# Kernel tuning notes

Measured on AMD Instinct MI355X. Metric: run time of the kernel, lower is better.

## Reference

```python
import jax, jax.numpy as jnp
import numpy as np

N = 50000   # nodes
E = 800000  # edges per timestep
T = 2
IN_C = 128
HID = 128


def gcn_conv(x, src, dst, W, b):
    """PyG GCNConv: add self-loops, symmetric normalization, linear, scatter-add, bias."""
    n = x.shape[0]
    loop = jnp.arange(n, dtype=src.dtype)
    s = jnp.concatenate([src, loop])  # [E+N]
    d = jnp.concatenate([dst, loop])
    h = x @ W                          # [N, H]
    deg = jax.ops.segment_sum(jnp.ones_like(d, dtype=x.dtype), d, num_segments=n)
    dinv = jnp.where(deg > 0, jax.lax.rsqrt(deg), 0.0)
    norm = dinv[s] * dinv[d]           # [E+N]
    msg = h[s] * norm[:, None]         # gather + scale
    out = jax.ops.segment_sum(msg, d, num_segments=n)  # scatter-add
    return out + b


def setup_inputs() -> dict:
    key = jax.random.key(0)
    ks = jax.random.split(key, 6)
    x_seq = jax.random.normal(ks[0], (T, N, IN_C), dtype=jnp.float32)
    edge_indices = jax.random.randint(ks[1], (T, 2, E), 0, N, dtype=jnp.int64)
    W1 = jax.random.normal(ks[2], (IN_C, HID), dtype=jnp.float32) * (1.0 / np.sqrt(IN_C))
    b1 = jnp.zeros((HID,), dtype=jnp.float32)
    W2 = jax.random.normal(ks[3], (HID, HID), dtype=jnp.float32) * (1.0 / np.sqrt(HID))
    b2 = jnp.zeros((HID,), dtype=jnp.float32)
    Wc = jax.random.normal(ks[4], (HID, 1), dtype=jnp.float32) * (1.0 / np.sqrt(HID))
    bc = jnp.zeros((1,), dtype=jnp.float32)
    return {"x_seq": x_seq, "edge_indices": edge_indices, "W1": W1, "b1": b1,
            "W2": W2, "b2": b2, "Wc": Wc, "bc": bc}


def reference(x_seq, edge_indices, W1, b1, W2, b2, Wc, bc):
    outputs = []
    for t in range(T):  # small fixed timestep loop, as in original
        x_t = x_seq[t]
        src = edge_indices[t, 0]
        dst = edge_indices[t, 1]
        h = jax.nn.relu(gcn_conv(x_t, src, dst, W1, b1))
        # dropout is inference-identity (eval mode)
        h = gcn_conv(h, src, dst, W2, b2)
        outputs.append(h)
    final = outputs[-1]
    importance_out = (final @ Wc + bc).squeeze(-1)  # [N]
    return (importance_out, *outputs)
```

## Files before the change

kernel.cpp:

```cpp
#include <hip/hip_runtime.h>
#include <hip/hip_bf16.h>

typedef unsigned int u32;
typedef unsigned short u16;
typedef unsigned long long u64;
typedef __bf16 bf16x8 __attribute__((ext_vector_type(8)));
typedef short short8 __attribute__((ext_vector_type(8)));
typedef float floatx4 __attribute__((ext_vector_type(4)));

__device__ inline float b2f(u16 b) { return __uint_as_float((u32)b << 16); }
__device__ inline float lo2f(u32 p) { return __uint_as_float(p << 16); }
__device__ inline float hi2f(u32 p) { return __uint_as_float(p & 0xffff0000u); }
__device__ inline u16 f2bs(float f) {
    __hip_bfloat16 h = __float2bfloat16(f);
    return *reinterpret_cast<u16*>(&h);
}
__device__ inline float ldext(const void* p, int fl, int i) {
    return fl ? ((const float*)p)[i] : b2f(((const u16*)p)[i]);
}

__global__ __launch_bounds__(64) void detect_kernel(const int* __restrict__ eb,
                                                    const u32* __restrict__ xw,
                                                    int* __restrict__ flags,
                                                    int S, int n) {
    __shared__ int sh[64 * 3];
    int lane = threadIdx.x & 63;
    int zc = 0, explo = 0;
#pragma unroll
    for (int r = 0; r < 4; ++r) {
        int i = 64 * r + lane;
        zc += (eb[2 * i + 1] == 0) ? 1 : 0;
        u32 w = xw[i];
        int e = (int)((w >> 7) & 0xFF);
        explo += (e >= 96 && e <= 140) ? 1 : 0;
    }
    sh[lane] = zc;
    sh[64 + lane] = explo;
    __syncthreads();
    int fl = 0;
    {
        int z = 0;
        for (int j = 0; j < 64; ++j) z += sh[j];
        fl = (z > 200) ? 1 : 0;
    }
    int vc = 0;
#pragma unroll
    for (int r = 0; r < 4; ++r) {
        int li = S / 2 + 64 * r + lane;
        int v = fl ? eb[2 * li] : eb[li];
        vc += ((unsigned)v < (unsigned)n) ? 1 : 0;
    }
    sh[128 + lane] = vc;
    __syncthreads();
    if (lane == 0) {
        int vtot = 0, etot = 0;
        for (int j = 0; j < 64; ++j) vtot += sh[128 + j];
        for (int j = 0; j < 64; ++j) etot += sh[64 + j];
        flags[0] = fl;
        flags[1] = (etot >= 192) ? 0 : 1;
        flags[2] = (vtot >= 240) ? (S / 4) : (S / 8);
    }
}

__device__ inline int load_edge(const int* eb, int fl, int idx) {
    return eb[fl ? (idx << 1) : idx];
}

#define PCHUNK 4096
__global__ __launch_bounds__(256) void part_kernel(const int* __restrict__ eb,
                                                   const int* __restrict__ flags,
                                                   int* __restrict__ bkcnt,
                                                   u64* __restrict__ pairs,
                                                   int n, int shift, int capP) {
    __shared__ int cnt[512];
    __shared__ int gbase[512];
    const int E = flags[2];
    const int fl = flags[0];
    const int nbuk = (2 * n + (1 << shift) - 1) >> shift;
    const int tid = threadIdx.x;
    for (int i = tid; i < nbuk; i += 256) cnt[i] = 0;
    __syncthreads();
    const int e0 = blockIdx.x * PCHUNK;
    u32 sv[16]; int gv[16], rk[16];
#pragma unroll
    for (int j = 0; j < 16; ++j) {
        int e = e0 + j * 256 + tid;
        u32 gs = 0; int g = -1;
        if (e < 2 * E) {
            int t = (e >= E) ? 1 : 0;
            int le = e - t * E;
            gs = (u32)(t * n) + (u32)load_edge(eb, fl, t * 2 * E + le);
            unsigned du = (unsigned)load_edge(eb, fl, t * 2 * E + E + le);
            if (du < (unsigned)n) g = t * n + (int)du;
        }
        sv[j] = gs;
        gv[j] = g;
        rk[j] = (g >= 0) ? atomicAdd(&cnt[g >> shift], 1) : 0;
    }
    __syncthreads();
    for (int b = tid; b < nbuk; b += 256) {
        int c = cnt[b];
        gbase[b] = c ? atomicAdd(&bkcnt[b], c) : 0;
    }
    __syncthreads();
#pragma unroll
    for (int j = 0; j < 16; ++j) {
        if (gv[j] >= 0) {
            int b = gv[j] >> shift;
            int idx = gbase[b] + rk[j];
            if (idx < capP)
                pairs[(size_t)b * capP + idx] =
                    ((u64)(u32)gv[j] << 32) | sv[j];
        }
    }
}

__global__ __launch_bounds__(256) void scat_kernel(const u64* __restrict__ pairs,
                                                   const int* __restrict__ bkcnt,
                                                   int* __restrict__ deg,
                                                   int* __restrict__ off,
                                                   float* __restrict__ dinv,
                                                   int* __restrict__ ssrc,
                                                   int n2, int shift, int capP) {
    __shared__ int hist[1024];
    __shared__ int lscan[256];
    const int b = blockIdx.x;
    const int d0 = b << shift;
    if (d0 >= n2) return;
    int nn = (1 << shift);
    if (d0 + nn > n2) nn = n2 - d0;
    const int tid = threadIdx.x;
    for (int j = tid; j < nn; j += 256) hist[j] = 0;
    __syncthreads();
    int cnt = bkcnt[b];
    if (cnt > capP) cnt = capP;
    const int gb = b * capP;
    const u64* pb = pairs + (size_t)gb;
    for (int i = tid; i < cnt; i += 256) {
        unsigned dl = (unsigned)(int)(pb[i] >> 32) - (unsigned)d0;
        if (dl < (unsigned)nn) atomicAdd(&hist[dl], 1);
    }
    __syncthreads();
    int base4 = tid * 4;
    int s0 = 0, s1 = 0, s2 = 0, s3 = 0;
    if (base4 < nn) {
        s0 = hist[base4];
        s1 = (base4 + 1 < nn) ? hist[base4 + 1] : 0;
        s2 = (base4 + 2 < nn) ? hist[base4 + 2] : 0;
        s3 = (base4 + 3 < nn) ? hist[base4 + 3] : 0;
    }
    int tsum = s0 + s1 + s2 + s3;
    lscan[tid] = tsum;
    __syncthreads();
    int val = tsum;
    for (int o = 1; o < 256; o <<= 1) {
        int add = (tid >= o) ? lscan[tid - o] : 0;
        __syncthreads();
        val += add;
        lscan[tid] = val;
        __syncthreads();
    }
    int texcl = val - tsum;
    if (base4 < nn) {
        int g = d0 + base4;
        int o0 = gb + texcl;
        deg[g] = s0; off[g] = o0; dinv[g] = rsqrtf((float)(s0 + 1));
        hist[base4] = o0;
        if (base4 + 1 < nn) {
            int o1 = o0 + s0;
            deg[g + 1] = s1; off[g + 1] = o1; dinv[g + 1] = rsqrtf((float)(s1 + 1));
            hist[base4 + 1] = o1;
        }
        if (base4 + 2 < nn) {
            int o2 = o0 + s0 + s1;
            deg[g + 2] = s2; off[g + 2] = o2; dinv[g + 2] = rsqrtf((float)(s2 + 1));
            hist[base4 + 2] = o2;
        }
        if (base4 + 3 < nn) {
            int o3 = o0 + s0 + s1 + s2;
            deg[g + 3] = s3; off[g + 3] = o3; dinv[g + 3] = rsqrtf((float)(s3 + 1));
            hist[base4 + 3] = o3;
        }
    }
    __syncthreads();
    const int limit = gb + cnt;
    for (int i = tid; i < cnt; i += 256) {
        u64 p = pb[i];
        unsigned dl = (unsigned)(int)(p >> 32) - (unsigned)d0;
        if (dl < (unsigned)nn) {
            int pos = atomicAdd(&hist[dl], 1);
            if (pos < limit) ssrc[pos] = (int)(u32)p;
        }
    }
}

__global__ __launch_bounds__(256) void prep_w(const void* __restrict__ W1,
                                              const void* __restrict__ W2,
                                              const int* __restrict__ flags,
                                              u16* __restrict__ W1t,
                                              u16* __restrict__ W2t) {
    int tid = blockIdx.x * 256 + threadIdx.x;
    if (tid < 2 * 128 * 128) {
        int which = tid >> 14;
        int r = tid & 16383;
        const void* W = which ? W2 : W1;
        u16* Wt = which ? W2t : W1t;
        int c = r >> 7, k = r & 127;
        Wt[c * 128 + k] = f2bs(ldext(W, flags[1], k * 128 + c));
    }
}

__global__ __launch_bounds__(256) void gemm_mfma(const void* __restrict__ Xv,
                                                 int x_ext,
                                                 const u16* __restrict__ Wt,
                                                 const int* __restrict__ flags,
                                                 const float* __restrict__ dinv,
                                                 u16* __restrict__ hs, int n) {
    __shared__ u16 Ws[128 * 136];
    {
        u32* wsu = (u32*)Ws;
        const u32* wtu = (const u32*)Wt;
        for (int i = threadIdx.x; i < 128 * 64; i += 256) {
            int c = i >> 6, kk = i & 63;
            wsu[c * 68 + kk] = wtu[i];
        }
    }
    __syncthreads();

    const int wave = threadIdx.x >> 6;
    const int lane = threadIdx.x & 63;
    const int m = lane & 15;
    const int quad = lane >> 4;
    const int node0 = blockIdx.x * 64 + wave * 16;
    if (node0 >= n) return;

    const int xf32 = x_ext ? flags[1] : 0;
    int va = node0 + m;
    if (va > n - 1) va = n - 1;

    floatx4 acc[8];
#pragma unroll
    for (int t = 0; t < 8; ++t) acc[t] = (floatx4){0.f, 0.f, 0.f, 0.f};

#pragma unroll
    for (int ks = 0; ks < 4; ++ks) {
        bf16x8 a;
        if (xf32) {
            const float* Xf = (const float*)Xv + (size_t)va * 128 + ks * 32 + quad * 8;
            float4 x0 = *(const float4*)Xf;
            float4 x1 = *(const float4*)(Xf + 4);
            short8 as;
            as[0] = (short)f2bs(x0.x); as[1] = (short)f2bs(x0.y);
            as[2] = (short)f2bs(x0.z); as[3] = (short)f2bs(x0.w);
            as[4] = (short)f2bs(x1.x); as[5] = (short)f2bs(x1.y);
            as[6] = (short)f2bs(x1.z); as[7] = (short)f2bs(x1.w);
            a = __builtin_bit_cast(bf16x8, as);
        } else {
            const u16* Xb = (const u16*)Xv + (size_t)va * 128 + ks * 32 + quad * 8;
            a = *(const bf16x8*)Xb;
        }
#pragma unroll
        for (int t = 0; t < 8; ++t) {
            const bf16x8 b = *(const bf16x8*)(Ws + (16 * t + m) * 136 + ks * 32 + quad * 8);
            acc[t] = __builtin_amdgcn_mfma_f32_16x16x32_bf16(a, b, acc[t], 0, 0, 0);
        }
    }

#pragma unroll
    for (int r = 0; r < 4; ++r) {
        int v = node0 + quad * 4 + r;
        if (v < n) {
            float dv = dinv[v];
#pragma unroll
            for (int t = 0; t < 8; ++t)
                hs[(size_t)v * 128 + 16 * t + m] = f2bs(acc[t][r] * dv);
        }
    }
}

__global__ __launch_bounds__(256) void gather_kernel(const u16* __restrict__ hs,
                                                     const int* __restrict__ off,
                                                     const int* __restrict__ deg,
                                                     const int* __restrict__ ssrc,
                                                     const float* __restrict__ dinv,
                                                     const void* __restrict__ bias,
                                                     const int* __restrict__ flags,
                                                     float* __restrict__ outf,
                                                     u16* __restrict__ outb,
                                                     const void* __restrict__ Wc,
                                                     const void* __restrict__ bc,
                                                     float* __restrict__ imp,
                                                     int n2, int half, int relu) {
    int w = (blockIdx.x * 256 + threadIdx.x) >> 6;
    int lane = threadIdx.x & 63;
    if (w >= n2) return;

    const u32* hsu = (const u32*)hs;
    u32 p = hsu[(size_t)w * 64 + lane];
    float ax = lo2f(p), ay = hi2f(p);
    int i = __builtin_amdgcn_readfirstlane(off[w]);
    int end = i + __builtin_amdgcn_readfirstlane(deg[w]);
    unsigned nm1 = (unsigned)(n2 - 1);

    float bx = 0.f, by = 0.f, cx = 0.f, cy = 0.f, dx = 0.f, dy = 0.f;
    for (; i + 8 <= end; i += 8) {
        unsigned s0 = (unsigned)ssrc[i];     if (s0 > nm1) s0 = 0;
        unsigned s1 = (unsigned)ssrc[i + 1]; if (s1 > nm1) s1 = 0;
        unsigned s2 = (unsigned)ssrc[i + 2]; if (s2 > nm1) s2 = 0;
        unsigned s3 = (unsigned)ssrc[i + 3]; if (s3 > nm1) s3 = 0;
        unsigned s4 = (unsigned)ssrc[i + 4]; if (s4 > nm1) s4 = 0;
        unsigned s5 = (unsigned)ssrc[i + 5]; if (s5 > nm1) s5 = 0;
        unsigned s6 = (unsigned)ssrc[i + 6]; if (s6 > nm1) s6 = 0;
        unsigned s7 = (unsigned)ssrc[i + 7]; if (s7 > nm1) s7 = 0;
        u32 v0 = hsu[(size_t)s0 * 64 + lane];
        u32 v1 = hsu[(size_t)s1 * 64 + lane];
        u32 v2 = hsu[(size_t)s2 * 64 + lane];
        u32 v3 = hsu[(size_t)s3 * 64 + lane];
        u32 v4 = hsu[(size_t)s4 * 64 + lane];
        u32 v5 = hsu[(size_t)s5 * 64 + lane];
        u32 v6 = hsu[(size_t)s6 * 64 + lane];
        u32 v7 = hsu[(size_t)s7 * 64 + lane];
        ax += lo2f(v0); ay += hi2f(v0);
        bx += lo2f(v1); by += hi2f(v1);
        cx += lo2f(v2); cy += hi2f(v2);
        dx += lo2f(v3); dy += hi2f(v3);
        ax += lo2f(v4); ay += hi2f(v4);
        bx += lo2f(v5); by += hi2f(v5);
        cx += lo2f(v6); cy += hi2f(v6);
        dx += lo2f(v7); dy += hi2f(v7);
    }
    for (; i + 4 <= end; i += 4) {
        unsigned s0 = (unsigned)ssrc[i];     if (s0 > nm1) s0 = 0;
        unsigned s1 = (unsigned)ssrc[i + 1]; if (s1 > nm1) s1 = 0;
        unsigned s2 = (unsigned)ssrc[i + 2]; if (s2 > nm1) s2 = 0;
        unsigned s3 = (unsigned)ssrc[i + 3]; if (s3 > nm1) s3 = 0;
        u32 v0 = hsu[(size_t)s0 * 64 + lane];
        u32 v1 = hsu[(size_t)s1 * 64 + lane];
        u32 v2 = hsu[(size_t)s2 * 64 + lane];
        u32 v3 = hsu[(size_t)s3 * 64 + lane];
        ax += lo2f(v0); ay += hi2f(v0);
        bx += lo2f(v1); by += hi2f(v1);
        cx += lo2f(v2); cy += hi2f(v2);
        dx += lo2f(v3); dy += hi2f(v3);
    }
    for (; i < end; ++i) {
        unsigned s = (unsigned)ssrc[i];
        if (s > nm1) s = 0;
        u32 v = hsu[(size_t)s * 64 + lane];
        ax += lo2f(v);
        ay += hi2f(v);
    }
    ax += bx + cx + dx;
    ay += by + cy + dy;

    int ffl = flags[1];
    float dv = dinv[w];
    float o0 = dv * ax + ldext(bias, ffl, 2 * lane);
    float o1 = dv * ay + ldext(bias, ffl, 2 * lane + 1);
    if (relu) {
        o0 = fmaxf(o0, 0.f);
        o1 = fmaxf(o1, 0.f);
    }
    if (outf) ((float2*)outf)[(size_t)w * 64 + lane] = make_float2(o0, o1);
    else ((u32*)outb)[(size_t)w * 64 + lane] = (u32)f2bs(o0) | ((u32)f2bs(o1) << 16);

    if (imp && w >= half) {
        float cb = o0 * ldext(Wc, ffl, 2 * lane) + o1 * ldext(Wc, ffl, 2 * lane + 1);
        cb += __shfl_xor(cb, 32);
        cb += __shfl_xor(cb, 16);
        cb += __shfl_xor(cb, 8);
        cb += __shfl_xor(cb, 4);
        cb += __shfl_xor(cb, 2);
        cb += __shfl_xor(cb, 1);
        if (lane == 0) imp[w - half] = cb + ldext(bc, ffl, 0);
    }
}

extern "C" void kernel_launch(void* const* d_in, const int* in_sizes, int n_in,
                              void* d_out, int out_size, void* d_ws, size_t ws_size,
                              hipStream_t stream) {
    const int T = 2, C = 128;
    const int N = in_sizes[0] / (T * C);
    const int S = in_sizes[1];
    const int Emax = S / 4;
    const int N2 = 2 * N;
    (void)Emax;

    const void* x_seq = d_in[0];
    const int* edges = (const int*)d_in[1];
    const void* W1 = d_in[2];
    const void* b1 = d_in[3];
    const void* W2 = d_in[4];
    const void* b2 = d_in[5];
    const void* Wc = d_in[6];
    const void* bc = d_in[7];

    float* out = (float*)d_out;
    float* R = out + N;

    char* p = (char*)d_ws;
    auto alloc = [&](size_t bytes) {
        char* r = p;
        p += (bytes + 255) & ~(size_t)255;
        return r;
    };
    int* flags = (int*)alloc(256);
    int* deg = (int*)alloc((size_t)N2 * 4);
    int* off = (int*)alloc((size_t)N2 * 4);
    float* dinv = (float*)alloc((size_t)N2 * 4);
    int* bkcnt = (int*)alloc(512 * 4);

    int shift = 8;
    while ((((N2 + (1 << shift) - 1) >> shift) > 512) && shift < 10) ++shift;
    const int NBUK = (N2 + (1 << shift) - 1) >> shift;
    const size_t aliasBytes = (size_t)2 * N2 * C * 2;
    const int capP = (int)(aliasBytes / (8 * (size_t)NBUK));

    int* ssrc = (int*)alloc((size_t)NBUK * capP * 4);
    u16* W1t = (u16*)alloc(128 * 128 * 2);
    u16* W2t = (u16*)alloc(128 * 128 * 2);
    u16* hsb = (u16*)alloc((size_t)N2 * C * 2);
    u16* hmb = (u16*)alloc((size_t)N2 * C * 2);
    u64* pairs = (u64*)hsb;

    const int gP = (2 * Emax + PCHUNK - 1) / PCHUNK;
    const int gN2 = (N2 + 3) / 4;
    const int gG2 = (N2 + 63) / 64;
    const int gW = (2 * 128 * 128 + 255) / 256;

    detect_kernel<<<1, 64, 0, stream>>>(edges, (const u32*)x_seq, flags, S, N);
    prep_w<<<gW, 256, 0, stream>>>(W1, W2, flags, W1t, W2t);

    hipMemsetAsync(bkcnt, 0, 512 * 4, stream);
    part_kernel<<<gP, 256, 0, stream>>>(edges, flags, bkcnt, pairs, N, shift, capP);
    scat_kernel<<<NBUK, 256, 0, stream>>>(pairs, bkcnt, deg, off, dinv,
                                          ssrc, N2, shift, capP);

    gemm_mfma<<<gG2, 256, 0, stream>>>(x_seq, 1, W1t, flags, dinv, hsb, N2);
    gather_kernel<<<gN2, 256, 0, stream>>>(hsb, off, deg, ssrc, dinv, b1, flags,
                                           (float*)nullptr, hmb,
                                           nullptr, nullptr, (float*)nullptr,
                                           N2, N, 1);

    gemm_mfma<<<gG2, 256, 0, stream>>>(hmb, 0, W2t, flags, dinv, hsb, N2);
    gather_kernel<<<gN2, 256, 0, stream>>>(hsb, off, deg, ssrc, dinv, b2, flags,
                                           R, (u16*)nullptr,
                                           Wc, bc, out,
                                           N2, N, 0);
}
```

Before: 293.2 us.

## Replace CSR adjacency with fixed 32-slot padded ELL plus overflow list

Neighbor lists become a fixed 32-slot-per-node ELL layout padded with a sentinel that maps to an all-zero row, with a separate overflow array for nodes of higher degree. The gather then loads all 32 indices at once with vector loads and issues 32 unconditional row loads, with no offset lookup or loop tail. Weight preparation moves into extra blocks of the partition kernel, and bucket-counter zeroing moves into the detect kernel, which removes a launch and a memset. The cost is wasted gathers on padded slots, since average degree is about 16, plus the extra work of writing sentinels.

```diff
diff --git a/kernel.cpp b/kernel.cpp
--- a/kernel.cpp
+++ b/kernel.cpp
@@ -8,6 +8,8 @@
 typedef short short8 __attribute__((ext_vector_type(8)));
 typedef float floatx4 __attribute__((ext_vector_type(4)));
 
+#define SENT 0x7FFFFFFF
+
 __device__ inline float b2f(u16 b) { return __uint_as_float((u32)b << 16); }
 __device__ inline float lo2f(u32 p) { return __uint_as_float(p << 16); }
 __device__ inline float hi2f(u32 p) { return __uint_as_float(p & 0xffff0000u); }
@@ -22,9 +24,13 @@
 __global__ __launch_bounds__(64) void detect_kernel(const int* __restrict__ eb,
                                                     const u32* __restrict__ xw,
                                                     int* __restrict__ flags,
+                                                    int* __restrict__ bkcnt,
+                                                    int* __restrict__ ovfcur,
                                                     int S, int n) {
     __shared__ int sh[64 * 3];
     int lane = threadIdx.x & 63;
+    for (int j = lane; j < 512; j += 64) bkcnt[j] = 0;
+    if (lane == 0) *ovfcur = 0;
     int zc = 0, explo = 0;
 #pragma unroll
     for (int r = 0; r < 4; ++r) {
@@ -71,9 +77,26 @@
                                                    const int* __restrict__ flags,
                                                    int* __restrict__ bkcnt,
                                                    u64* __restrict__ pairs,
-                                                   int n, int shift, int capP) {
+                                                   int n, int shift, int capP,
+                                                   int gP,
+                                                   const void* __restrict__ W1,
+                                                   const void* __restrict__ W2,
+                                                   u16* __restrict__ W1t,
+                                                   u16* __restrict__ W2t) {
     __shared__ int cnt[512];
     __shared__ int gbase[512];
+    if ((int)blockIdx.x >= gP) {
+        int tid = (blockIdx.x - gP) * 256 + threadIdx.x;
+        if (tid < 2 * 128 * 128) {
+            int which = tid >> 14;
+            int r = tid & 16383;
+            const void* W = which ? W2 : W1;
+            u16* Wt = which ? W2t : W1t;
+            int c = r >> 7, k = r & 127;
+            Wt[c * 128 + k] = f2bs(ldext(W, flags[1], k * 128 + c));
+        }
+        return;
+    }
     const int E = flags[2];
     const int fl = flags[0];
     const int nbuk = (2 * n + (1 << shift) - 1) >> shift;
@@ -118,95 +141,51 @@
 __global__ __launch_bounds__(256) void scat_kernel(const u64* __restrict__ pairs,
                                                    const int* __restrict__ bkcnt,
                                                    int* __restrict__ deg,
-                                                   int* __restrict__ off,
                                                    float* __restrict__ dinv,
                                                    int* __restrict__ ssrc,
+                                                   int* __restrict__ ovf,
+                                                   int* __restrict__ ovfoff,
+                                                   int* __restrict__ ovfcur,
                                                    int n2, int shift, int capP) {
     __shared__ int hist[1024];
-    __shared__ int lscan[256];
+    __shared__ int cur[1024];
     const int b = blockIdx.x;
     const int d0 = b << shift;
     if (d0 >= n2) return;
     int nn = (1 << shift);
     if (d0 + nn > n2) nn = n2 - d0;
     const int tid = threadIdx.x;
-    for (int j = tid; j < nn; j += 256) hist[j] = 0;
+    for (int j = tid; j < nn; j += 256) { hist[j] = 0; cur[j] = 0; }
     __syncthreads();
     int cnt = bkcnt[b];
     if (cnt > capP) cnt = capP;
-    const int gb = b * capP;
-    const u64* pb = pairs + (size_t)gb;
+    const u64* pb = pairs + (size_t)b * capP;
     for (int i = tid; i < cnt; i += 256) {
         unsigned dl = (unsigned)(int)(pb[i] >> 32) - (unsigned)d0;
         if (dl < (unsigned)nn) atomicAdd(&hist[dl], 1);
     }
     __syncthreads();
-    int base4 = tid * 4;
-    int s0 = 0, s1 = 0, s2 = 0, s3 = 0;
-    if (base4 < nn) {
-        s0 = hist[base4];
-        s1 = (base4 + 1 < nn) ? hist[base4 + 1] : 0;
-        s2 = (base4 + 2 < nn) ? hist[base4 + 2] : 0;
-        s3 = (base4 + 3 < nn) ? hist[base4 + 3] : 0;
-    }
-    int tsum = s0 + s1 + s2 + s3;
-    lscan[tid] = tsum;
-    __syncthreads();
-    int val = tsum;
-    for (int o = 1; o < 256; o <<= 1) {
-        int add = (tid >= o) ? lscan[tid - o] : 0;
-        __syncthreads();
-        val += add;
-        lscan[tid] = val;
-        __syncthreads();
-    }
-    int texcl = val - tsum;
-    if (base4 < nn) {
-        int g = d0 + base4;
-        int o0 = gb + texcl;
-        deg[g] = s0; off[g] = o0; dinv[g] = rsqrtf((float)(s0 + 1));
-        hist[base4] = o0;
-        if (base4 + 1 < nn) {
-            int o1 = o0 + s0;
-            deg[g + 1] = s1; off[g + 1] = o1; dinv[g + 1] = rsqrtf((float)(s1 + 1));
-            hist[base4 + 1] = o1;
-        }
-        if (base4 + 2 < nn) {
-            int o2 = o0 + s0 + s1;
-            deg[g + 2] = s2; off[g + 2] = o2; dinv[g + 2] = rsqrtf((float)(s2 + 1));
-            hist[base4 + 2] = o2;
-        }
-        if (base4 + 3 < nn) {
-            int o3 = o0 + s0 + s1 + s2;
-            deg[g + 3] = s3; off[g + 3] = o3; dinv[g + 3] = rsqrtf((float)(s3 + 1));
-            hist[base4 + 3] = o3;
-        }
-    }
-    __syncthreads();
-    const int limit = gb + cnt;
+    for (int j = tid; j < nn; j += 256) {
+        int d = hist[j];
+        int g = d0 + j;
+        deg[g] = d;
+        dinv[g] = rsqrtf((float)(d + 1));
+        if (d > 32) ovfoff[g] = atomicAdd(ovfcur, d - 32);
+    }
+    for (int idx = tid; idx < nn * 32; idx += 256) {
+        int node = idx >> 5, slot = idx & 31;
+        if (slot >= hist[node]) ssrc[(size_t)(d0 + node) * 32 + slot] = SENT;
+    }
+    __syncthreads();
     for (int i = tid; i < cnt; i += 256) {
         u64 p = pb[i];
         unsigned dl = (unsigned)(int)(p >> 32) - (unsigned)d0;
         if (dl < (unsigned)nn) {
-            int pos = atomicAdd(&hist[dl], 1);
-            if (pos < limit) ssrc[pos] = (int)(u32)p;
-        }
-    }
-}
-
-__global__ __launch_bounds__(256) void prep_w(const void* __restrict__ W1,
-                                              const void* __restrict__ W2,
-                                              const int* __restrict__ flags,
-                                              u16* __restrict__ W1t,
-                                              u16* __restrict__ W2t) {
-    int tid = blockIdx.x * 256 + threadIdx.x;
-    if (tid < 2 * 128 * 128) {
-        int which = tid >> 14;
-        int r = tid & 16383;
-        const void* W = which ? W2 : W1;
-        u16* Wt = which ? W2t : W1t;
-        int c = r >> 7, k = r & 127;
-        Wt[c * 128 + k] = f2bs(ldext(W, flags[1], k * 128 + c));
+            int g = d0 + (int)dl;
+            int slot = atomicAdd(&cur[dl], 1);
+            if (slot < 32) ssrc[(size_t)g * 32 + slot] = (int)(u32)p;
+            else ovf[ovfoff[g] + slot - 32] = (int)(u32)p;
+        }
     }
 }
 
@@ -216,6 +195,8 @@
                                                  const int* __restrict__ flags,
                                                  const float* __restrict__ dinv,
                                                  u16* __restrict__ hs, int n) {
+    if (blockIdx.x == 0 && threadIdx.x < 64)
+        ((u32*)hs)[(size_t)n * 64 + threadIdx.x] = 0;
     __shared__ u16 Ws[128 * 136];
     {
         u32* wsu = (u32*)Ws;
@@ -279,9 +260,10 @@
 }
 
 __global__ __launch_bounds__(256) void gather_kernel(const u16* __restrict__ hs,
-                                                     const int* __restrict__ off,
                                                      const int* __restrict__ deg,
                                                      const int* __restrict__ ssrc,
+                                                     const int* __restrict__ ovf,
+                                                     const int* __restrict__ ovfoff,
                                                      const float* __restrict__ dinv,
                                                      const void* __restrict__ bias,
                                                      const int* __restrict__ flags,
@@ -291,70 +273,92 @@
                                                      const void* __restrict__ bc,
                                                      float* __restrict__ imp,
                                                      int n2, int half, int relu) {
-    int w = (blockIdx.x * 256 + threadIdx.x) >> 6;
-    int lane = threadIdx.x & 63;
+    const int lane = threadIdx.x & 63;
+    int w = __builtin_amdgcn_readfirstlane((blockIdx.x * 256 + threadIdx.x) >> 6);
     if (w >= n2) return;
 
     const u32* hsu = (const u32*)hs;
-    u32 p = hsu[(size_t)w * 64 + lane];
-    float ax = lo2f(p), ay = hi2f(p);
-    int i = __builtin_amdgcn_readfirstlane(off[w]);
-    int end = i + __builtin_amdgcn_readfirstlane(deg[w]);
-    unsigned nm1 = (unsigned)(n2 - 1);
-
+    const unsigned nm1 = (unsigned)(n2 - 1);
+    const unsigned zrow = (unsigned)n2;
+
+    const int dg = __builtin_amdgcn_readfirstlane(deg[w]);
+    const int* sp = ssrc + (size_t)w * 32;
+
+    int4 q0 = *(const int4*)(sp);
+    int4 q1 = *(const int4*)(sp + 4);
+    int4 q2 = *(const int4*)(sp + 8);
+    int4 q3 = *(const int4*)(sp + 12);
+    int4 q4 = *(const int4*)(sp + 16);
+    int4 q5 = *(const int4*)(sp + 20);
+    int4 q6 = *(const int4*)(sp + 24);
+    int4 q7 = *(const int4*)(sp + 28);
+    u32 pself = hsu[(size_t)w * 64 + lane];
+
+#define CLAMP(x) ((unsigned)(x) > nm1 ? zrow : (unsigned)(x))
+    unsigned s00 = CLAMP(q0.x), s01 = CLAMP(q0.y), s02 = CLAMP(q0.z), s03 = CLAMP(q0.w);
+    unsigned s04 = CLAMP(q1.x), s05 = CLAMP(q1.y), s06 = CLAMP(q1.z), s07 = CLAMP(q1.w);
+    unsigned s08 = CLAMP(q2.x), s09 = CLAMP(q2.y), s10 = CLAMP(q2.z), s11 = CLAMP(q2.w);
+    unsigned s12 = CLAMP(q3.x), s13 = CLAMP(q3.y), s14 = CLAMP(q3.z), s15 = CLAMP(q3.w);
+    unsigned s16 = CLAMP(q4.x), s17 = CLAMP(q4.y), s18 = CLAMP(q4.z), s19 = CLAMP(q4.w);
+    unsigned s20 = CLAMP(q5.x), s21 = CLAMP(q5.y), s22 = CLAMP(q5.z), s23 = CLAMP(q5.w);
+    unsigned s24 = CLAMP(q6.x), s25 = CLAMP(q6.y), s26 = CLAMP(q6.z), s27 = CLAMP(q6.w);
+    unsigned s28 = CLAMP(q7.x), s29 = CLAMP(q7.y), s30 = CLAMP(q7.z), s31 = CLAMP(q7.w);
+#undef CLAMP
+
+    float ax = lo2f(pself), ay = hi2f(pself);
     float bx = 0.f, by = 0.f, cx = 0.f, cy = 0.f, dx = 0.f, dy = 0.f;
-    for (; i + 8 <= end; i += 8) {
-        unsigned s0 = (unsigned)ssrc[i];     if (s0 > nm1) s0 = 0;
-        unsigned s1 = (unsigned)ssrc[i + 1]; if (s1 > nm1) s1 = 0;
-        unsigned s2 = (unsigned)ssrc[i + 2]; if (s2 > nm1) s2 = 0;
-        unsigned s3 = (unsigned)ssrc[i + 3]; if (s3 > nm1) s3 = 0;
-        unsigned s4 = (unsigned)ssrc[i + 4]; if (s4 > nm1) s4 = 0;
-        unsigned s5 = (unsigned)ssrc[i + 5]; if (s5 > nm1) s5 = 0;
-        unsigned s6 = (unsigned)ssrc[i + 6]; if (s6 > nm1) s6 = 0;
-        unsigned s7 = (unsigned)ssrc[i + 7]; if (s7 > nm1) s7 = 0;
-        u32 v0 = hsu[(size_t)s0 * 64 + lane];
-        u32 v1 = hsu[(size_t)s1 * 64 + lane];
-        u32 v2 = hsu[(size_t)s2 * 64 + lane];
-        u32 v3 = hsu[(size_t)s3 * 64 + lane];
-        u32 v4 = hsu[(size_t)s4 * 64 + lane];
-        u32 v5 = hsu[(size_t)s5 * 64 + lane];
-        u32 v6 = hsu[(size_t)s6 * 64 + lane];
-        u32 v7 = hsu[(size_t)s7 * 64 + lane];
-        ax += lo2f(v0); ay += hi2f(v0);
-        bx += lo2f(v1); by += hi2f(v1);
-        cx += lo2f(v2); cy += hi2f(v2);
-        dx += lo2f(v3); dy += hi2f(v3);
-        ax += lo2f(v4); ay += hi2f(v4);
-        bx += lo2f(v5); by += hi2f(v5);
-        cx += lo2f(v6); cy += hi2f(v6);
-        dx += lo2f(v7); dy += hi2f(v7);
-    }
-    for (; i + 4 <= end; i += 4) {
-        unsigned s0 = (unsigned)ssrc[i];     if (s0 > nm1) s0 = 0;
-        unsigned s1 = (unsigned)ssrc[i + 1]; if (s1 > nm1) s1 = 0;
-        unsigned s2 = (unsigned)ssrc[i + 2]; if (s2 > nm1) s2 = 0;
-        unsigned s3 = (unsigned)ssrc[i + 3]; if (s3 > nm1) s3 = 0;
-        u32 v0 = hsu[(size_t)s0 * 64 + lane];
-        u32 v1 = hsu[(size_t)s1 * 64 + lane];
-        u32 v2 = hsu[(size_t)s2 * 64 + lane];
-        u32 v3 = hsu[(size_t)s3 * 64 + lane];
-        ax += lo2f(v0); ay += hi2f(v0);
-        bx += lo2f(v1); by += hi2f(v1);
-        cx += lo2f(v2); cy += hi2f(v2);
-        dx += lo2f(v3); dy += hi2f(v3);
-    }
-    for (; i < end; ++i) {
-        unsigned s = (unsigned)ssrc[i];
-        if (s > nm1) s = 0;
-        u32 v = hsu[(size_t)s * 64 + lane];
-        ax += lo2f(v);
-        ay += hi2f(v);
-    }
+
+#define ROW(s) hsu[(size_t)(s) * 64 + lane]
+    {
+        u32 v0 = ROW(s00), v1 = ROW(s01), v2 = ROW(s02), v3 = ROW(s03);
+        u32 v4 = ROW(s04), v5 = ROW(s05), v6 = ROW(s06), v7 = ROW(s07);
+        ax += lo2f(v0); ay += hi2f(v0);  bx += lo2f(v1); by += hi2f(v1);
+        cx += lo2f(v2); cy += hi2f(v2);  dx += lo2f(v3); dy += hi2f(v3);
+        ax += lo2f(v4); ay += hi2f(v4);  bx += lo2f(v5); by += hi2f(v5);
+        cx += lo2f(v6); cy += hi2f(v6);  dx += lo2f(v7); dy += hi2f(v7);
+    }
+    {
+        u32 v0 = ROW(s08), v1 = ROW(s09), v2 = ROW(s10), v3 = ROW(s11);
+        u32 v4 = ROW(s12), v5 = ROW(s13), v6 = ROW(s14), v7 = ROW(s15);
+        ax += lo2f(v0); ay += hi2f(v0);  bx += lo2f(v1); by += hi2f(v1);
+        cx += lo2f(v2); cy += hi2f(v2);  dx += lo2f(v3); dy += hi2f(v3);
+        ax += lo2f(v4); ay += hi2f(v4);  bx += lo2f(v5); by += hi2f(v5);
+        cx += lo2f(v6); cy += hi2f(v6);  dx += lo2f(v7); dy += hi2f(v7);
+    }
+    {
+        u32 v0 = ROW(s16), v1 = ROW(s17), v2 = ROW(s18), v3 = ROW(s19);
+        u32 v4 = ROW(s20), v5 = ROW(s21), v6 = ROW(s22), v7 = ROW(s23);
+        ax += lo2f(v0); ay += hi2f(v0);  bx += lo2f(v1); by += hi2f(v1);
+        cx += lo2f(v2); cy += hi2f(v2);  dx += lo2f(v3); dy += hi2f(v3);
+        ax += lo2f(v4); ay += hi2f(v4);  bx += lo2f(v5); by += hi2f(v5);
+        cx += lo2f(v6); cy += hi2f(v6);  dx += lo2f(v7); dy += hi2f(v7);
+    }
+    {
+        u32 v0 = ROW(s24), v1 = ROW(s25), v2 = ROW(s26), v3 = ROW(s27);
+        u32 v4 = ROW(s28), v5 = ROW(s29), v6 = ROW(s30), v7 = ROW(s31);
+        ax += lo2f(v0); ay += hi2f(v0);  bx += lo2f(v1); by += hi2f(v1);
+        cx += lo2f(v2); cy += hi2f(v2);  dx += lo2f(v3); dy += hi2f(v3);
+        ax += lo2f(v4); ay += hi2f(v4);  bx += lo2f(v5); by += hi2f(v5);
+        cx += lo2f(v6); cy += hi2f(v6);  dx += lo2f(v7); dy += hi2f(v7);
+    }
+
+    if (dg > 32) {
+        int ob = __builtin_amdgcn_readfirstlane(ovfoff[w]);
+        int cnt = dg - 32;
+        for (int j = 0; j < cnt; ++j) {
+            unsigned s = (unsigned)ovf[ob + j];
+            if (s > nm1) s = zrow;
+            u32 v = ROW(s);
+            ax += lo2f(v); ay += hi2f(v);
+        }
+    }
+#undef ROW
+
     ax += bx + cx + dx;
     ay += by + cy + dy;
 
-    int ffl = flags[1];
-    float dv = dinv[w];
+    const int ffl = flags[1];
+    const float dv = dinv[w];
     float o0 = dv * ax + ldext(bias, ffl, 2 * lane);
     float o1 = dv * ay + ldext(bias, ffl, 2 * lane + 1);
     if (relu) {
@@ -384,7 +388,6 @@
     const int S = in_sizes[1];
     const int Emax = S / 4;
     const int N2 = 2 * N;
-    (void)Emax;
 
     const void* x_seq = d_in[0];
     const int* edges = (const int*)d_in[1];
@@ -406,45 +409,47 @@
     };
     int* flags = (int*)alloc(256);
     int* deg = (int*)alloc((size_t)N2 * 4);
-    int* off = (int*)alloc((size_t)N2 * 4);
     float* dinv = (float*)alloc((size_t)N2 * 4);
     int* bkcnt = (int*)alloc(512 * 4);
+    int* ovfcur = (int*)alloc(256);
+    int* ovfoff = (int*)alloc((size_t)N2 * 4);
 
     int shift = 8;
     while ((((N2 + (1 << shift) - 1) >> shift) > 512) && shift < 10) ++shift;
     const int NBUK = (N2 + (1 << shift) - 1) >> shift;
     const size_t aliasBytes = (size_t)2 * N2 * C * 2;
-    const int capP = (int)(aliasBytes / (8 * (size_t)NBUK));
-
-    int* ssrc = (int*)alloc((size_t)NBUK * capP * 4);
+    const int capP = (int)(aliasBytes / (8 * (size_t)NBUK)) & ~3;
+
+    int* ssrc = (int*)alloc((size_t)N2 * 32 * 4);
+    int* ovf = (int*)alloc((size_t)2 * Emax * 4);
     u16* W1t = (u16*)alloc(128 * 128 * 2);
     u16* W2t = (u16*)alloc(128 * 128 * 2);
-    u16* hsb = (u16*)alloc((size_t)N2 * C * 2);
+    u16* hsb = (u16*)alloc((size_t)(N2 + 2) * C * 2);
     u16* hmb = (u16*)alloc((size_t)N2 * C * 2);
     u64* pairs = (u64*)hsb;
 
     const int gP = (2 * Emax + PCHUNK - 1) / PCHUNK;
-    const int gN2 = (N2 + 3) / 4;
+    const int gW = (2 * 128 * 128 + 255) / 256;
+    const int gGA = (N2 + 3) / 4;
     const int gG2 = (N2 + 63) / 64;
-    const int gW = (2 * 128 * 128 + 255) / 256;
-
-    detect_kernel<<<1, 64, 0, stream>>>(edges, (const u32*)x_seq, flags, S, N);
-    prep_w<<<gW, 256, 0, stream>>>(W1, W2, flags, W1t, W2t);
-
-    hipMemsetAsync(bkcnt, 0, 512 * 4, stream);
-    part_kernel<<<gP, 256, 0, stream>>>(edges, flags, bkcnt, pairs, N, shift, capP);
-    scat_kernel<<<NBUK, 256, 0, stream>>>(pairs, bkcnt, deg, off, dinv,
-                                          ssrc, N2, shift, capP);
+
+    detect_kernel<<<1, 64, 0, stream>>>(edges, (const u32*)x_seq, flags, bkcnt,
+                                        ovfcur, S, N);
+
+    part_kernel<<<gP + gW, 256, 0, stream>>>(edges, flags, bkcnt, pairs, N, shift,
+                                             capP, gP, W1, W2, W1t, W2t);
+    scat_kernel<<<NBUK, 256, 0, stream>>>(pairs, bkcnt, deg, dinv, ssrc,
+                                          ovf, ovfoff, ovfcur, N2, shift, capP);
 
     gemm_mfma<<<gG2, 256, 0, stream>>>(x_seq, 1, W1t, flags, dinv, hsb, N2);
-    gather_kernel<<<gN2, 256, 0, stream>>>(hsb, off, deg, ssrc, dinv, b1, flags,
-                                           (float*)nullptr, hmb,
+    gather_kernel<<<gGA, 256, 0, stream>>>(hsb, deg, ssrc, ovf, ovfoff, dinv, b1,
+                                           flags, (float*)nullptr, hmb,
                                            nullptr, nullptr, (float*)nullptr,
                                            N2, N, 1);
 
     gemm_mfma<<<gG2, 256, 0, stream>>>(hmb, 0, W2t, flags, dinv, hsb, N2);
-    gather_kernel<<<gN2, 256, 0, stream>>>(hsb, off, deg, ssrc, dinv, b2, flags,
-                                           R, (u16*)nullptr,
+    gather_kernel<<<gGA, 256, 0, stream>>>(hsb, deg, ssrc, ovf, ovfoff, dinv, b2,
+                                           flags, R, (u16*)nullptr,
                                            Wc, bc, out,
                                            N2, N, 0);
 }
```

Result: faster. 284.4 us (-3.0%).
